# Kernel tuning notes

Measured on AMD Instinct MI355X. Metric: run time of the kernel, lower is better.

## Reference

```python
import jax, jax.numpy as jnp
import numpy as np

N, E, D, T = 10000, 320000, 128, 128


def _layer_norm(x, g, b, eps=1e-5):
    mu = jnp.mean(x, axis=-1, keepdims=True)
    var = jnp.mean(jnp.square(x - mu), axis=-1, keepdims=True)
    return (x - mu) * jax.lax.rsqrt(var + eps) * g + b


def setup_inputs() -> dict:
    key = jax.random.key(0)
    ks = jax.random.split(key, 24)
    s = 0.05

    def lin(k, fin, fout):
        k1, k2 = jax.random.split(k)
        return (jax.random.normal(k1, (fin, fout), jnp.float32) * s,
                jax.random.normal(k2, (fout,), jnp.float32) * s)

    W_tp, b_tp = lin(ks[5], T, D)
    W_sg, b_sg = lin(ks[6], D, D)
    W_dg, b_dg = lin(ks[7], D, D)
    W_eg, b_eg = lin(ks[8], D, D)
    W_su, b_su = lin(ks[9], D, D)
    W_du, b_du = lin(ks[10], D, D)
    return {
        'node_feats': jax.random.normal(ks[0], (N, D), jnp.float32),
        'edge_feats': jax.random.normal(ks[1], (E, D), jnp.float32),
        'time_feats': jax.random.normal(ks[2], (N, T), jnp.float32),
        'src': jax.random.randint(ks[3], (E,), 0, N),
        'dst': jax.random.randint(ks[4], (E,), 0, N),
        'W_tp': W_tp, 'b_tp': b_tp,
        'W_sg': W_sg, 'b_sg': b_sg,
        'W_dg': W_dg, 'b_dg': b_dg,
        'W_eg': W_eg, 'b_eg': b_eg,
        'W_su': W_su, 'b_su': b_su,
        'W_du': W_du, 'b_du': b_du,
        'ln_e_g': jnp.ones((D,), jnp.float32), 'ln_e_b': jnp.zeros((D,), jnp.float32),
        'ln_n_g': jnp.ones((D,), jnp.float32), 'ln_n_b': jnp.zeros((D,), jnp.float32),
    }


def reference(node_feats, edge_feats, time_feats, src, dst,
              W_tp, b_tp, W_sg, b_sg, W_dg, b_dg, W_eg, b_eg,
              W_su, b_su, W_du, b_du, ln_e_g, ln_e_b, ln_n_g, ln_n_b):
    n_nodes = node_feats.shape[0]
    # per-node gate projections (time proj folded into source gate)
    e_src = node_feats @ W_sg + b_sg + time_feats @ W_tp + b_tp   # [N, D]
    e_dst = node_feats @ W_dg + b_dg                              # [N, D]
    # edge gating: gather from both endpoints + edge feature projection
    m = e_src[src] + e_dst[dst] + edge_feats @ W_eg + b_eg        # [E, D]
    sigma = jax.nn.sigmoid(m)                                     # [E, D]
    # gated message passing: scatter-add over destination nodes
    Bh = node_feats @ W_du + b_du                                 # [N, D]
    sum_sigma_h = jax.ops.segment_sum(Bh[src] * sigma, dst, num_segments=n_nodes)
    sum_sigma = jax.ops.segment_sum(sigma, dst, num_segments=n_nodes)
    h = sum_sigma_h / (sum_sigma + 1e-6)                          # [N, D]
    x = node_feats @ W_su + b_su + h
    x = jax.nn.silu(_layer_norm(x, ln_n_g, ln_n_b))
    y = jax.nn.silu(_layer_norm(m, ln_e_g, ln_e_b))
    x = node_feats + x  # residual
    y = edge_feats + y
    return (x, y)
```

## Files before the change

### kernel.cpp

```cpp
#include <hip/hip_runtime.h>
#include <hip/hip_bf16.h>

#define N_NODES 10000
#define N_EDGES 320000
#define D 128
#define NBINS 10000

typedef float f32x4 __attribute__((ext_vector_type(4)));
typedef float f32x2 __attribute__((ext_vector_type(2)));
typedef short bf16x8 __attribute__((ext_vector_type(8)));

static __device__ inline short f2bf(float f) {
    union { __hip_bfloat16 h; short s; } u;
    u.h = __float2bfloat16(f);
    return u.s;
}

static __device__ inline float bf2f(short s) {
    union { float f; unsigned u; } x;
    x.u = ((unsigned)(unsigned short)s) << 16;
    return x.f;
}

static __device__ inline float fast_rcp(float x) { return __builtin_amdgcn_rcpf(x); }

__global__ void prepack_all(const float* __restrict__ W_sg, const float* __restrict__ W_tp,
                            const float* __restrict__ W_dg, const float* __restrict__ W_du,
                            const float* __restrict__ W_su, const float* __restrict__ W_eg,
                            short* __restrict__ Wsrc, short* __restrict__ Wdg,
                            short* __restrict__ Wdu, short* __restrict__ Wsu,
                            short* __restrict__ Weg) {
    int idx = blockIdx.x * 256 + threadIdx.x;
    const float* W0; const float* W1; short* out; int i2;
    if (idx < 32768)      { W0 = W_sg; W1 = W_tp; out = Wsrc; i2 = idx; }
    else if (idx < 49152) { W0 = W_dg; W1 = W_dg; out = Wdg;  i2 = idx - 32768; }
    else if (idx < 65536) { W0 = W_du; W1 = W_du; out = Wdu;  i2 = idx - 49152; }
    else if (idx < 81920) { W0 = W_su; W1 = W_su; out = Wsu;  i2 = idx - 65536; }
    else                  { W0 = W_eg; W1 = W_eg; out = Weg;  i2 = idx - 81920; }
    int b  = i2 & 7;
    int l  = (i2 >> 3) & 63;
    int jt = (i2 >> 9) & 7;
    int t  = i2 >> 12;
    int k = 32 * t + ((l >> 4) * 8) + b;
    int j = jt * 16 + (l & 15);
    float v = (k < 128) ? W0[k * 128 + j] : W1[(k - 128) * 128 + j];
    out[i2] = f2bf(v);
}

__global__ void hist_kernel(const int* __restrict__ dst, int* __restrict__ cnt) {
    int i = blockIdx.x * 256 + threadIdx.x;
    if (i < N_EDGES) atomicAdd(&cnt[dst[i]], 1);
}

__launch_bounds__(1024)
__global__ void scan_kernel(const int* __restrict__ cnt, int* __restrict__ cursor) {
    __shared__ int s[1024];
    int t = threadIdx.x;
    int b0 = t * 10;
    int loc[10];
    int tot = 0;
#pragma unroll
    for (int i = 0; i < 10; ++i) {
        int v = (b0 + i < NBINS) ? cnt[b0 + i] : 0;
        loc[i] = tot; tot += v;
    }
    s[t] = tot;
    __syncthreads();
    for (int off = 1; off < 1024; off <<= 1) {
        int v = (t >= off) ? s[t - off] : 0;
        __syncthreads();
        s[t] += v;
        __syncthreads();
    }
    int base = (t == 0) ? 0 : s[t - 1];
#pragma unroll
    for (int i = 0; i < 10; ++i)
        if (b0 + i < NBINS) cursor[b0 + i] = base + loc[i];
}

__global__ void scatter_kernel(const int* __restrict__ src, const int* __restrict__ dst,
                               int* __restrict__ cursor,
                               int* __restrict__ perm,
                               int* __restrict__ src_s, int* __restrict__ dst_s) {
    int i = blockIdx.x * 256 + threadIdx.x;
    if (i < N_EDGES) {
        int d = dst[i];
        int p = atomicAdd(&cursor[d], 1);
        perm[p] = i;
        src_s[p] = src[i];
        dst_s[p] = d;
    }
}

__launch_bounds__(256)
__global__ void node_proj_kernel(const float* __restrict__ node,
                                 const float* __restrict__ timef,
                                 const short* __restrict__ Wsrc_pk,
                                 const short* __restrict__ Wdg_pk,
                                 const short* __restrict__ Wdu_pk,
                                 const short* __restrict__ Wsu_pk,
                                 const float* __restrict__ b_sg, const float* __restrict__ b_tp,
                                 const float* __restrict__ b_dg, const float* __restrict__ b_du,
                                 const float* __restrict__ b_su, const float* __restrict__ b_eg,
                                 short* __restrict__ spk,
                                 short* __restrict__ dpk,
                                 float* __restrict__ xs) {
    int tid = threadIdx.x;
    int w = tid >> 6;
    int l = tid & 63;
    int g = l >> 4;
    int lr = l & 15;
    int r0 = blockIdx.x * 64 + w * 16;
    int arow = r0 + lr;

    bf16x8 aN[4], aT[4];
    if (arow < N_NODES) {
        const float* np = node + (size_t)arow * D;
        const float* tp = timef + (size_t)arow * D;
#pragma unroll
        for (int t = 0; t < 4; ++t) {
            int k0 = 32 * t + g * 8;
            f32x4 v0 = *(const f32x4*)(np + k0);
            f32x4 v1 = *(const f32x4*)(np + k0 + 4);
            f32x4 u0 = *(const f32x4*)(tp + k0);
            f32x4 u1 = *(const f32x4*)(tp + k0 + 4);
            bf16x8 a, b;
#pragma unroll
            for (int i = 0; i < 4; ++i) {
                a[i] = f2bf(v0[i]); a[4 + i] = f2bf(v1[i]);
                b[i] = f2bf(u0[i]); b[4 + i] = f2bf(u1[i]);
            }
            aN[t] = a; aT[t] = b;
        }
    } else {
        bf16x8 z = {0, 0, 0, 0, 0, 0, 0, 0};
#pragma unroll
        for (int t = 0; t < 4; ++t) { aN[t] = z; aT[t] = z; }
    }

    const bf16x8* Bsrc = (const bf16x8*)Wsrc_pk;
    const bf16x8* Bdg  = (const bf16x8*)Wdg_pk;
    const bf16x8* Bdu  = (const bf16x8*)Wdu_pk;
    const bf16x8* Bsu  = (const bf16x8*)Wsu_pk;

    {
        bf16x8 chunk[4];
#pragma unroll
        for (int jt = 0; jt < 8; ++jt) {
            int c = jt * 16 + lr;
            f32x4 acc = {0.f, 0.f, 0.f, 0.f};
#pragma unroll
            for (int t = 0; t < 4; ++t)
                acc = __builtin_amdgcn_mfma_f32_16x16x32_bf16(aN[t], Bsrc[(t * 8 + jt) * 64 + l], acc, 0, 0, 0);
#pragma unroll
            for (int t = 0; t < 4; ++t)
                acc = __builtin_amdgcn_mfma_f32_16x16x32_bf16(aT[t], Bsrc[((4 + t) * 8 + jt) * 64 + l], acc, 0, 0, 0);
            float bias = b_sg[c] + b_tp[c];
#pragma unroll
            for (int r = 0; r < 4; ++r) chunk[r][jt] = f2bf(acc[r] + bias);
        }
#pragma unroll
        for (int r = 0; r < 4; ++r) {
            int row = r0 + g * 4 + r;
            if (row < N_NODES) *(bf16x8*)(spk + (size_t)row * 256 + lr * 8) = chunk[r];
        }
    }

    {
        bf16x8 chD[4], chH[4];
        float xsv[4][8];
#pragma unroll
        for (int jt = 0; jt < 8; ++jt) {
            int c = jt * 16 + lr;
            f32x4 a0 = {0.f, 0.f, 0.f, 0.f}, a1 = a0, a2 = a0;
#pragma unroll
            for (int t = 0; t < 4; ++t) {
                a0 = __builtin_amdgcn_mfma_f32_16x16x32_bf16(aN[t], Bdg[(t * 8 + jt) * 64 + l], a0, 0, 0, 0);
                a1 = __builtin_amdgcn_mfma_f32_16x16x32_bf16(aN[t], Bdu[(t * 8 + jt) * 64 + l], a1, 0, 0, 0);
                a2 = __builtin_amdgcn_mfma_f32_16x16x32_bf16(aN[t], Bsu[(t * 8 + jt) * 64 + l], a2, 0, 0, 0);
            }
            float bdgc = b_dg[c] + b_eg[c];
            float bdu = b_du[c], bsu = b_su[c];
#pragma unroll
            for (int r = 0; r < 4; ++r) {
                chD[r][jt] = f2bf(a0[r] + bdgc);
                chH[r][jt] = f2bf(a1[r] + bdu);
                xsv[r][jt] = a2[r] + bsu;
            }
        }
#pragma unroll
        for (int r = 0; r < 4; ++r) {
            int row = r0 + g * 4 + r;
            if (row < N_NODES) {
                *(bf16x8*)(dpk + (size_t)row * D + lr * 8) = chD[r];
                *(bf16x8*)(spk + (size_t)row * 256 + 128 + lr * 8) = chH[r];
#pragma unroll
                for (int jt = 0; jt < 8; ++jt)
                    xs[(size_t)row * D + jt * 16 + lr] = xsv[r][jt];
            }
        }
    }
}

__launch_bounds__(256)
__global__ void edge_kernel(const float* __restrict__ edgef,
                            const int* __restrict__ perm,
                            const int* __restrict__ src_s, const int* __restrict__ dst_s,
                            const short* __restrict__ Weg_pk,
                            const short* __restrict__ spk,
                            const short* __restrict__ dpk,
                            const float* __restrict__ ln_g, const float* __restrict__ ln_b,
                            float* __restrict__ ss, float* __restrict__ ssh,
                            float* __restrict__ y) {
    __shared__ short Bs[128 * 128];
    {
        const bf16x8* gw = (const bf16x8*)Weg_pk;
        bf16x8* sw = (bf16x8*)Bs;
        for (int i = threadIdx.x; i < 2048; i += 256) sw[i] = gw[i];
    }
    __syncthreads();

    int tid = threadIdx.x;
    int w = tid >> 6;
    int l = tid & 63;
    int g = l >> 4;
    int lr = l & 15;
    int b = blockIdx.x;
    int swz = (b & 7) * 625 + (b >> 3);
    int e0 = swz * 64 + w * 16;

    int eA = perm[e0 + lr];
    int eidx[4], sidx[4], didx[4];
#pragma unroll
    for (int r = 0; r < 4; ++r) {
        eidx[r] = perm[e0 + g * 4 + r];
        sidx[r] = src_s[e0 + g * 4 + r];
        didx[r] = dst_s[e0 + g * 4 + r];
    }

    bf16x8 esv[4], bhv[4], edv[4];
#pragma unroll
    for (int r = 0; r < 4; ++r) {
        esv[r] = *(const bf16x8*)(spk + (size_t)sidx[r] * 256 + lr * 8);
        bhv[r] = *(const bf16x8*)(spk + (size_t)sidx[r] * 256 + 128 + lr * 8);
        edv[r] = *(const bf16x8*)(dpk + (size_t)didx[r] * D + lr * 8);
    }

    bf16x8 aE[4];
    {
        const float* ep = edgef + (size_t)eA * D;
#pragma unroll
        for (int t = 0; t < 4; ++t) {
            int k0 = 32 * t + g * 8;
            f32x4 v0 = *(const f32x4*)(ep + k0);
            f32x4 v1 = *(const f32x4*)(ep + k0 + 4);
            bf16x8 a;
#pragma unroll
            for (int i = 0; i < 4; ++i) { a[i] = f2bf(v0[i]); a[4 + i] = f2bf(v1[i]); }
            aE[t] = a;
        }
    }

    const bf16x8* Bp = (const bf16x8*)Bs;
    f32x4 acc[8];
#pragma unroll
    for (int jt = 0; jt < 8; ++jt) {
        f32x4 c4 = {0.f, 0.f, 0.f, 0.f};
#pragma unroll
        for (int t = 0; t < 4; ++t)
            c4 = __builtin_amdgcn_mfma_f32_16x16x32_bf16(aE[t], Bp[(t * 8 + jt) * 64 + l], c4, 0, 0, 0);
        acc[jt] = c4;
    }

    int dfirst = __shfl(didx[0], 0);
    int dlast  = __shfl(didx[3], 48);
    bool uniform = (dfirst == dlast);

    float sum[4] = {0.f, 0.f, 0.f, 0.f}, sq[4] = {0.f, 0.f, 0.f, 0.f};
#pragma unroll
    for (int jt = 0; jt < 8; ++jt) {
        int c = jt * 16 + lr;
        float sg[4], bsg[4];
#pragma unroll
        for (int r = 0; r < 4; ++r) {
            float m = acc[jt][r] + bf2f(esv[r][jt]) + bf2f(edv[r][jt]);
            acc[jt][r] = m;
            float s = fast_rcp(1.f + __expf(-m));
            sg[r] = s;
            bsg[r] = bf2f(bhv[r][jt]) * s;
            sum[r] += m; sq[r] += m * m;
        }
        if (uniform) {
            float aS = (sg[0] + sg[1]) + (sg[2] + sg[3]);
            float aH = (bsg[0] + bsg[1]) + (bsg[2] + bsg[3]);
            aS += __shfl_xor(aS, 16); aH += __shfl_xor(aH, 16);
            aS += __shfl_xor(aS, 32); aH += __shfl_xor(aH, 32);
            if (g == 0) {
                atomicAdd(&ss [(size_t)dfirst * D + c], aS);
                atomicAdd(&ssh[(size_t)dfirst * D + c], aH);
            }
        } else {
            float aS = sg[0], aH = bsg[0];
#pragma unroll
            for (int r = 1; r < 4; ++r) {
                if (didx[r] == didx[r - 1]) { aS += sg[r]; aH += bsg[r]; }
                else {
                    atomicAdd(&ss [(size_t)didx[r - 1] * D + c], aS);
                    atomicAdd(&ssh[(size_t)didx[r - 1] * D + c], aH);
                    aS = sg[r]; aH = bsg[r];
                }
            }
            atomicAdd(&ss [(size_t)didx[3] * D + c], aS);
            atomicAdd(&ssh[(size_t)didx[3] * D + c], aH);
        }
    }

#pragma unroll
    for (int r = 0; r < 4; ++r) {
        float s = sum[r], q = sq[r];
#pragma unroll
        for (int mk = 1; mk < 16; mk <<= 1) { s += __shfl_xor(s, mk); q += __shfl_xor(q, mk); }
        float mean = s * (1.f / D);
        float var = q * (1.f / D) - mean * mean;
        sum[r] = mean;
        sq[r] = rsqrtf(var + 1e-5f);
    }

#pragma unroll
    for (int jt = 0; jt < 8; ++jt) {
        int c = jt * 16 + lr;
        float gc = ln_g[c], bc = ln_b[c];
#pragma unroll
        for (int r = 0; r < 4; ++r) {
            float v = (acc[jt][r] - sum[r]) * sq[r] * gc + bc;
            float sl = v * fast_rcp(1.f + __expf(-v));
            size_t off = (size_t)eidx[r] * D + c;
            __builtin_nontemporal_store(edgef[off] + sl, &y[off]);
        }
    }
}

__launch_bounds__(256)
__global__ void node_out_kernel(const float* __restrict__ node,
                                const float* __restrict__ xs,
                                const float* __restrict__ ssh, const float* __restrict__ ss,
                                const float* __restrict__ ln_g, const float* __restrict__ ln_b,
                                float* __restrict__ x) {
    int w = threadIdx.x >> 6;
    int l = threadIdx.x & 63;
    int row = blockIdx.x * 4 + w;
    if (row >= N_NODES) return;
    size_t base = (size_t)row * D + 2 * l;
    f32x2 xv = *(const f32x2*)(xs + base);
    f32x2 hs = *(const f32x2*)(ssh + base);
    f32x2 sv = *(const f32x2*)(ss + base);
    float v0 = xv[0] + hs[0] / (sv[0] + 1e-6f);
    float v1 = xv[1] + hs[1] / (sv[1] + 1e-6f);
    float s = v0 + v1, q = v0 * v0 + v1 * v1;
#pragma unroll
    for (int mk = 1; mk < 64; mk <<= 1) { s += __shfl_xor(s, mk); q += __shfl_xor(q, mk); }
    float mean = s * (1.f / D);
    float var = q * (1.f / D) - mean * mean;
    float rstd = rsqrtf(var + 1e-5f);
    float t0 = (v0 - mean) * rstd * ln_g[2 * l] + ln_b[2 * l];
    float t1 = (v1 - mean) * rstd * ln_g[2 * l + 1] + ln_b[2 * l + 1];
    t0 = t0 * fast_rcp(1.f + __expf(-t0));
    t1 = t1 * fast_rcp(1.f + __expf(-t1));
    f32x2 nv = *(const f32x2*)(node + base);
    f32x2 outv;
    outv[0] = nv[0] + t0;
    outv[1] = nv[1] + t1;
    *(f32x2*)(x + base) = outv;
}

extern "C" void kernel_launch(void* const* d_in, const int* in_sizes, int n_in,
                              void* d_out, int out_size, void* d_ws, size_t ws_size,
                              hipStream_t stream) {
    const float* node  = (const float*)d_in[0];
    const float* edgef = (const float*)d_in[1];
    const float* timef = (const float*)d_in[2];
    const int*   src   = (const int*)d_in[3];
    const int*   dst   = (const int*)d_in[4];
    const float* W_tp = (const float*)d_in[5];  const float* b_tp = (const float*)d_in[6];
    const float* W_sg = (const float*)d_in[7];  const float* b_sg = (const float*)d_in[8];
    const float* W_dg = (const float*)d_in[9];  const float* b_dg = (const float*)d_in[10];
    const float* W_eg = (const float*)d_in[11]; const float* b_eg = (const float*)d_in[12];
    const float* W_su = (const float*)d_in[13]; const float* b_su = (const float*)d_in[14];
    const float* W_du = (const float*)d_in[15]; const float* b_du = (const float*)d_in[16];
    const float* ln_e_g = (const float*)d_in[17]; const float* ln_e_b = (const float*)d_in[18];
    const float* ln_n_g = (const float*)d_in[19]; const float* ln_n_b = (const float*)d_in[20];

    char* ws = (char*)d_ws;
    size_t nd = (size_t)N_NODES * D;
    float* ss    = (float*)ws; ws += nd * 4;
    float* ssh   = (float*)ws; ws += nd * 4;
    float* xs    = (float*)ws; ws += nd * 4;
    short* spk   = (short*)ws; ws += (size_t)N_NODES * 256 * 2;
    short* dpk   = (short*)ws; ws += nd * 2;
    short* Wsrc_pk = (short*)ws; ws += 256 * 128 * 2;
    short* Wdg_pk  = (short*)ws; ws += 128 * 128 * 2;
    short* Wdu_pk  = (short*)ws; ws += 128 * 128 * 2;
    short* Wsu_pk  = (short*)ws; ws += 128 * 128 * 2;
    short* Weg_pk  = (short*)ws; ws += 128 * 128 * 2;
    int* cnt       = (int*)ws; ws += 10240 * 4;
    int* cursor    = (int*)ws; ws += 10240 * 4;
    int* perm      = (int*)ws; ws += (size_t)N_EDGES * 4;
    int* src_s     = (int*)ws; ws += (size_t)N_EDGES * 4;
    int* dst_s     = (int*)ws; ws += (size_t)N_EDGES * 4;

    hipMemsetAsync(ss, 0, 2 * nd * 4, stream);
    hipMemsetAsync(cnt, 0, 10240 * 4, stream);

    hist_kernel<<<(N_EDGES + 255) / 256, 256, 0, stream>>>(dst, cnt);
    scan_kernel<<<1, 1024, 0, stream>>>(cnt, cursor);
    scatter_kernel<<<(N_EDGES + 255) / 256, 256, 0, stream>>>(src, dst, cursor, perm, src_s, dst_s);

    prepack_all<<<384, 256, 0, stream>>>(W_sg, W_tp, W_dg, W_du, W_su, W_eg,
                                         Wsrc_pk, Wdg_pk, Wdu_pk, Wsu_pk, Weg_pk);

    node_proj_kernel<<<(N_NODES + 63) / 64, 256, 0, stream>>>(
        node, timef, Wsrc_pk, Wdg_pk, Wdu_pk, Wsu_pk,
        b_sg, b_tp, b_dg, b_du, b_su, b_eg, spk, dpk, xs);

    edge_kernel<<<N_EDGES / 64, 256, 0, stream>>>(
        edgef, perm, src_s, dst_s, Weg_pk, spk, dpk,
        ln_e_g, ln_e_b, ss, ssh, (float*)d_out + nd);

    node_out_kernel<<<N_NODES / 4, 256, 0, stream>>>(
        node, xs, ssh, ss, ln_n_g, ln_n_b, (float*)d_out);
}
```

Baseline: 245.2 us.

## Process two edge tiles per wave with interleaved gathers, fuse hist/prepack/memset

Each wave in the edge kernel now handles two 16-edge tiles and interleaves the second tile's gathers and edge-feature loads with the first tile's MFMA and epilogue, to hide gather latency. The grid halves and uses a new XCD-aware block swizzle. The source-gate and Bh rows are interleaved in spk so one 32-byte load fetches both. The histogram is fused with weight prepacking into one launch, and zeroing ss/ssh moves into node_proj, removing a memset and a kernel launch. The cost is higher register pressure from holding two tiles, which may reduce occupancy.

```diff
diff --git a/kernel.cpp b/kernel.cpp
--- a/kernel.cpp
+++ b/kernel.cpp
@@ -9,6 +9,7 @@
 typedef float f32x4 __attribute__((ext_vector_type(4)));
 typedef float f32x2 __attribute__((ext_vector_type(2)));
 typedef short bf16x8 __attribute__((ext_vector_type(8)));
+typedef short bf16x16 __attribute__((ext_vector_type(16)));
 
 static __device__ inline short f2bf(float f) {
     union { __hip_bfloat16 h; short s; } u;
@@ -24,13 +25,20 @@
 
 static __device__ inline float fast_rcp(float x) { return __builtin_amdgcn_rcpf(x); }
 
-__global__ void prepack_all(const float* __restrict__ W_sg, const float* __restrict__ W_tp,
-                            const float* __restrict__ W_dg, const float* __restrict__ W_du,
-                            const float* __restrict__ W_su, const float* __restrict__ W_eg,
-                            short* __restrict__ Wsrc, short* __restrict__ Wdg,
-                            short* __restrict__ Wdu, short* __restrict__ Wsu,
-                            short* __restrict__ Weg) {
-    int idx = blockIdx.x * 256 + threadIdx.x;
+__global__ void prep_hist(const float* __restrict__ W_sg, const float* __restrict__ W_tp,
+                          const float* __restrict__ W_dg, const float* __restrict__ W_du,
+                          const float* __restrict__ W_su, const float* __restrict__ W_eg,
+                          short* __restrict__ Wsrc, short* __restrict__ Wdg,
+                          short* __restrict__ Wdu, short* __restrict__ Wsu,
+                          short* __restrict__ Weg,
+                          const int* __restrict__ dst, int* __restrict__ cnt) {
+    int bid = blockIdx.x;
+    if (bid < 1250) {
+        int i = bid * 256 + threadIdx.x;
+        atomicAdd(&cnt[dst[i]], 1);
+        return;
+    }
+    int idx = (bid - 1250) * 256 + threadIdx.x;
     const float* W0; const float* W1; short* out; int i2;
     if (idx < 32768)      { W0 = W_sg; W1 = W_tp; out = Wsrc; i2 = idx; }
     else if (idx < 49152) { W0 = W_dg; W1 = W_dg; out = Wdg;  i2 = idx - 32768; }
@@ -47,11 +55,6 @@
     out[i2] = f2bf(v);
 }
 
-__global__ void hist_kernel(const int* __restrict__ dst, int* __restrict__ cnt) {
-    int i = blockIdx.x * 256 + threadIdx.x;
-    if (i < N_EDGES) atomicAdd(&cnt[dst[i]], 1);
-}
-
 __launch_bounds__(1024)
 __global__ void scan_kernel(const int* __restrict__ cnt, int* __restrict__ cursor) {
     __shared__ int s[1024];
@@ -104,7 +107,18 @@
                                  const float* __restrict__ b_su, const float* __restrict__ b_eg,
                                  short* __restrict__ spk,
                                  short* __restrict__ dpk,
-                                 float* __restrict__ xs) {
+                                 float* __restrict__ xs,
+                                 float* __restrict__ ss, float* __restrict__ ssh) {
+    {
+        int r0b = blockIdx.x * 64;
+        int nrows = N_NODES - r0b; if (nrows > 64) nrows = 64;
+        f32x4 z = {0.f, 0.f, 0.f, 0.f};
+        f32x4* s4 = (f32x4*)(ss + (size_t)r0b * D);
+        f32x4* h4 = (f32x4*)(ssh + (size_t)r0b * D);
+        int nch = nrows * D / 4;
+        for (int i = threadIdx.x; i < nch; i += 256) { s4[i] = z; h4[i] = z; }
+    }
+
     int tid = threadIdx.x;
     int w = tid >> 6;
     int l = tid & 63;
@@ -162,7 +176,7 @@
 #pragma unroll
         for (int r = 0; r < 4; ++r) {
             int row = r0 + g * 4 + r;
-            if (row < N_NODES) *(bf16x8*)(spk + (size_t)row * 256 + lr * 8) = chunk[r];
+            if (row < N_NODES) *(bf16x8*)(spk + (size_t)row * 256 + lr * 16) = chunk[r];
         }
     }
 
@@ -193,7 +207,7 @@
             int row = r0 + g * 4 + r;
             if (row < N_NODES) {
                 *(bf16x8*)(dpk + (size_t)row * D + lr * 8) = chD[r];
-                *(bf16x8*)(spk + (size_t)row * 256 + 128 + lr * 8) = chH[r];
+                *(bf16x8*)(spk + (size_t)row * 256 + lr * 16 + 8) = chH[r];
 #pragma unroll
                 for (int jt = 0; jt < 8; ++jt)
                     xs[(size_t)row * D + jt * 16 + lr] = xsv[r][jt];
@@ -201,6 +215,104 @@
         }
     }
 }
+
+
+#define TILE_LOAD_IDX(S, E0) \
+    const int eA##S = perm[(E0) + lr]; \
+    int eidx##S[4], sidx##S[4], didx##S[4]; \
+    _Pragma("unroll") \
+    for (int r = 0; r < 4; ++r) { \
+        int p = (E0) + g * 4 + r; \
+        eidx##S[r] = perm[p]; sidx##S[r] = src_s[p]; didx##S[r] = dst_s[p]; \
+    } \
+    const int df##S = __shfl(didx##S[0], 0); \
+    const bool uni##S = (df##S == __shfl(didx##S[3], 48));
+
+#define TILE_GATHER(S) \
+    bf16x16 esbh##S[4]; bf16x8 edv##S[4]; \
+    _Pragma("unroll") \
+    for (int r = 0; r < 4; ++r) \
+        esbh##S[r] = *(const bf16x16*)(spk + (size_t)sidx##S[r] * 256 + lr * 16); \
+    edv##S[0] = *(const bf16x8*)(dpk + (size_t)didx##S[0] * D + lr * 8); \
+    if (!uni##S) { \
+        _Pragma("unroll") \
+        for (int r = 1; r < 4; ++r) \
+            edv##S[r] = *(const bf16x8*)(dpk + (size_t)didx##S[r] * D + lr * 8); \
+    } else { edv##S[1] = edv##S[0]; edv##S[2] = edv##S[0]; edv##S[3] = edv##S[0]; }
+
+#define TILE_AFRAG(S) \
+    bf16x8 aE##S[4]; \
+    { const float* ep = edgef + (size_t)eA##S * D; \
+      _Pragma("unroll") \
+      for (int t = 0; t < 4; ++t) { \
+        int k0 = 32 * t + g * 8; \
+        f32x4 v0 = *(const f32x4*)(ep + k0); \
+        f32x4 v1 = *(const f32x4*)(ep + k0 + 4); \
+        bf16x8 a; \
+        _Pragma("unroll") \
+        for (int i = 0; i < 4; ++i) { a[i] = f2bf(v0[i]); a[4 + i] = f2bf(v1[i]); } \
+        aE##S[t] = a; } }
+
+#define TILE_COMPUTE(S) \
+    f32x4 acc##S[8]; \
+    _Pragma("unroll") \
+    for (int jt = 0; jt < 8; ++jt) { \
+        f32x4 c4 = {0.f, 0.f, 0.f, 0.f}; \
+        _Pragma("unroll") \
+        for (int t = 0; t < 4; ++t) \
+            c4 = __builtin_amdgcn_mfma_f32_16x16x32_bf16(aE##S[t], Bp[(t * 8 + jt) * 64 + l], c4, 0, 0, 0); \
+        acc##S[jt] = c4; } \
+    float sum##S[4] = {0.f, 0.f, 0.f, 0.f}, sq##S[4] = {0.f, 0.f, 0.f, 0.f}; \
+    _Pragma("unroll") \
+    for (int jt = 0; jt < 8; ++jt) { \
+        int c = jt * 16 + lr; \
+        float sg[4], bsg[4]; \
+        _Pragma("unroll") \
+        for (int r = 0; r < 4; ++r) { \
+            float m = acc##S[jt][r] + bf2f(esbh##S[r][jt]) + bf2f(edv##S[r][jt]); \
+            acc##S[jt][r] = m; \
+            float s = fast_rcp(1.f + __expf(-m)); \
+            sg[r] = s; bsg[r] = bf2f(esbh##S[r][8 + jt]) * s; \
+            sum##S[r] += m; sq##S[r] += m * m; } \
+        if (uni##S) { \
+            float aS = (sg[0] + sg[1]) + (sg[2] + sg[3]); \
+            float aH = (bsg[0] + bsg[1]) + (bsg[2] + bsg[3]); \
+            aS += __shfl_xor(aS, 16); aH += __shfl_xor(aH, 16); \
+            aS += __shfl_xor(aS, 32); aH += __shfl_xor(aH, 32); \
+            if (g == 0) { \
+                atomicAdd(&ss [(size_t)df##S * D + c], aS); \
+                atomicAdd(&ssh[(size_t)df##S * D + c], aH); } \
+        } else { \
+            float aS = sg[0], aH = bsg[0]; \
+            _Pragma("unroll") \
+            for (int r = 1; r < 4; ++r) { \
+                if (didx##S[r] == didx##S[r - 1]) { aS += sg[r]; aH += bsg[r]; } \
+                else { \
+                    atomicAdd(&ss [(size_t)didx##S[r - 1] * D + c], aS); \
+                    atomicAdd(&ssh[(size_t)didx##S[r - 1] * D + c], aH); \
+                    aS = sg[r]; aH = bsg[r]; } } \
+            atomicAdd(&ss [(size_t)didx##S[3] * D + c], aS); \
+            atomicAdd(&ssh[(size_t)didx##S[3] * D + c], aH); } }
+
+#define TILE_EPILOGUE(S) \
+    _Pragma("unroll") \
+    for (int r = 0; r < 4; ++r) { \
+        float s = sum##S[r], q = sq##S[r]; \
+        _Pragma("unroll") \
+        for (int mk = 1; mk < 16; mk <<= 1) { s += __shfl_xor(s, mk); q += __shfl_xor(q, mk); } \
+        float mean = s * (1.f / D); \
+        sum##S[r] = mean; \
+        sq##S[r] = rsqrtf(q * (1.f / D) - mean * mean + 1e-5f); } \
+    _Pragma("unroll") \
+    for (int jt = 0; jt < 8; ++jt) { \
+        int c = jt * 16 + lr; \
+        float gc = ln_g[c], bc = ln_b[c]; \
+        _Pragma("unroll") \
+        for (int r = 0; r < 4; ++r) { \
+            float v = (acc##S[jt][r] - sum##S[r]) * sq##S[r] * gc + bc; \
+            float sl = v * fast_rcp(1.f + __expf(-v)); \
+            size_t off = (size_t)eidx##S[r] * D + c; \
+            y[off] = __builtin_nontemporal_load(&edgef[off]) + sl; } }
 
 __launch_bounds__(256)
 __global__ void edge_kernel(const float* __restrict__ edgef,
@@ -225,119 +337,25 @@
     int l = tid & 63;
     int g = l >> 4;
     int lr = l & 15;
+
     int b = blockIdx.x;
-    int swz = (b & 7) * 625 + (b >> 3);
-    int e0 = swz * 64 + w * 16;
-
-    int eA = perm[e0 + lr];
-    int eidx[4], sidx[4], didx[4];
-#pragma unroll
-    for (int r = 0; r < 4; ++r) {
-        eidx[r] = perm[e0 + g * 4 + r];
-        sidx[r] = src_s[e0 + g * 4 + r];
-        didx[r] = dst_s[e0 + g * 4 + r];
-    }
-
-    bf16x8 esv[4], bhv[4], edv[4];
-#pragma unroll
-    for (int r = 0; r < 4; ++r) {
-        esv[r] = *(const bf16x8*)(spk + (size_t)sidx[r] * 256 + lr * 8);
-        bhv[r] = *(const bf16x8*)(spk + (size_t)sidx[r] * 256 + 128 + lr * 8);
-        edv[r] = *(const bf16x8*)(dpk + (size_t)didx[r] * D + lr * 8);
-    }
-
-    bf16x8 aE[4];
-    {
-        const float* ep = edgef + (size_t)eA * D;
-#pragma unroll
-        for (int t = 0; t < 4; ++t) {
-            int k0 = 32 * t + g * 8;
-            f32x4 v0 = *(const f32x4*)(ep + k0);
-            f32x4 v1 = *(const f32x4*)(ep + k0 + 4);
-            bf16x8 a;
-#pragma unroll
-            for (int i = 0; i < 4; ++i) { a[i] = f2bf(v0[i]); a[4 + i] = f2bf(v1[i]); }
-            aE[t] = a;
-        }
-    }
+    const int q = 312, rr = 4;
+    int xcd = b & 7, boff = b >> 3;
+    int swz = (xcd < rr ? xcd * (q + 1) : rr * (q + 1) + (xcd - rr) * q) + boff;
+    int ebase = swz * 128 + w * 32;
 
     const bf16x8* Bp = (const bf16x8*)Bs;
-    f32x4 acc[8];
-#pragma unroll
-    for (int jt = 0; jt < 8; ++jt) {
-        f32x4 c4 = {0.f, 0.f, 0.f, 0.f};
-#pragma unroll
-        for (int t = 0; t < 4; ++t)
-            c4 = __builtin_amdgcn_mfma_f32_16x16x32_bf16(aE[t], Bp[(t * 8 + jt) * 64 + l], c4, 0, 0, 0);
-        acc[jt] = c4;
-    }
-
-    int dfirst = __shfl(didx[0], 0);
-    int dlast  = __shfl(didx[3], 48);
-    bool uniform = (dfirst == dlast);
-
-    float sum[4] = {0.f, 0.f, 0.f, 0.f}, sq[4] = {0.f, 0.f, 0.f, 0.f};
-#pragma unroll
-    for (int jt = 0; jt < 8; ++jt) {
-        int c = jt * 16 + lr;
-        float sg[4], bsg[4];
-#pragma unroll
-        for (int r = 0; r < 4; ++r) {
-            float m = acc[jt][r] + bf2f(esv[r][jt]) + bf2f(edv[r][jt]);
-            acc[jt][r] = m;
-            float s = fast_rcp(1.f + __expf(-m));
-            sg[r] = s;
-            bsg[r] = bf2f(bhv[r][jt]) * s;
-            sum[r] += m; sq[r] += m * m;
-        }
-        if (uniform) {
-            float aS = (sg[0] + sg[1]) + (sg[2] + sg[3]);
-            float aH = (bsg[0] + bsg[1]) + (bsg[2] + bsg[3]);
-            aS += __shfl_xor(aS, 16); aH += __shfl_xor(aH, 16);
-            aS += __shfl_xor(aS, 32); aH += __shfl_xor(aH, 32);
-            if (g == 0) {
-                atomicAdd(&ss [(size_t)dfirst * D + c], aS);
-                atomicAdd(&ssh[(size_t)dfirst * D + c], aH);
-            }
-        } else {
-            float aS = sg[0], aH = bsg[0];
-#pragma unroll
-            for (int r = 1; r < 4; ++r) {
-                if (didx[r] == didx[r - 1]) { aS += sg[r]; aH += bsg[r]; }
-                else {
-                    atomicAdd(&ss [(size_t)didx[r - 1] * D + c], aS);
-                    atomicAdd(&ssh[(size_t)didx[r - 1] * D + c], aH);
-                    aS = sg[r]; aH = bsg[r];
-                }
-            }
-            atomicAdd(&ss [(size_t)didx[3] * D + c], aS);
-            atomicAdd(&ssh[(size_t)didx[3] * D + c], aH);
-        }
-    }
-
-#pragma unroll
-    for (int r = 0; r < 4; ++r) {
-        float s = sum[r], q = sq[r];
-#pragma unroll
-        for (int mk = 1; mk < 16; mk <<= 1) { s += __shfl_xor(s, mk); q += __shfl_xor(q, mk); }
-        float mean = s * (1.f / D);
-        float var = q * (1.f / D) - mean * mean;
-        sum[r] = mean;
-        sq[r] = rsqrtf(var + 1e-5f);
-    }
-
-#pragma unroll
-    for (int jt = 0; jt < 8; ++jt) {
-        int c = jt * 16 + lr;
-        float gc = ln_g[c], bc = ln_b[c];
-#pragma unroll
-        for (int r = 0; r < 4; ++r) {
-            float v = (acc[jt][r] - sum[r]) * sq[r] * gc + bc;
-            float sl = v * fast_rcp(1.f + __expf(-v));
-            size_t off = (size_t)eidx[r] * D + c;
-            __builtin_nontemporal_store(edgef[off] + sl, &y[off]);
-        }
-    }
+
+    TILE_LOAD_IDX(0, ebase)
+    TILE_LOAD_IDX(1, ebase + 16)
+    TILE_GATHER(0)
+    TILE_AFRAG(0)
+    TILE_AFRAG(1)
+    TILE_COMPUTE(0)
+    TILE_GATHER(1)
+    TILE_EPILOGUE(0)
+    TILE_COMPUTE(1)
+    TILE_EPILOGUE(1)
 }
 
 __launch_bounds__(256)
@@ -408,21 +426,19 @@
     int* src_s     = (int*)ws; ws += (size_t)N_EDGES * 4;
     int* dst_s     = (int*)ws; ws += (size_t)N_EDGES * 4;
 
-    hipMemsetAsync(ss, 0, 2 * nd * 4, stream);
     hipMemsetAsync(cnt, 0, 10240 * 4, stream);
 
-    hist_kernel<<<(N_EDGES + 255) / 256, 256, 0, stream>>>(dst, cnt);
+    prep_hist<<<1634, 256, 0, stream>>>(W_sg, W_tp, W_dg, W_du, W_su, W_eg,
+                                        Wsrc_pk, Wdg_pk, Wdu_pk, Wsu_pk, Weg_pk,
+                                        dst, cnt);
     scan_kernel<<<1, 1024, 0, stream>>>(cnt, cursor);
     scatter_kernel<<<(N_EDGES + 255) / 256, 256, 0, stream>>>(src, dst, cursor, perm, src_s, dst_s);
 
-    prepack_all<<<384, 256, 0, stream>>>(W_sg, W_tp, W_dg, W_du, W_su, W_eg,
-                                         Wsrc_pk, Wdg_pk, Wdu_pk, Wsu_pk, Weg_pk);
-
     node_proj_kernel<<<(N_NODES + 63) / 64, 256, 0, stream>>>(
         node, timef, Wsrc_pk, Wdg_pk, Wdu_pk, Wsu_pk,
-        b_sg, b_tp, b_dg, b_du, b_su, b_eg, spk, dpk, xs);
-
-    edge_kernel<<<N_EDGES / 64, 256, 0, stream>>>(
+        b_sg, b_tp, b_dg, b_du, b_su, b_eg, spk, dpk, xs, ss, ssh);
+
+    edge_kernel<<<2500, 256, 0, stream>>>(
         edgef, perm, src_s, dst_s, Weg_pk, spk, dpk,
         ln_e_g, ln_e_b, ss, ssh, (float*)d_out + nd);
 
```

New measurement: 256.4 us. 4.6% more time.
